# Kernel optimization log

Measured on AMD Instinct MI355X. Metric: run time of the kernel, lower is better.

The kernel has to match this reference:

```python
import jax, jax.numpy as jnp
import numpy as np

N = 4096        # batch size (rows)
K = 4           # instances per class -> num_instances in the torch code
D = 256         # embedding dim
MARGIN = 0.5
SAMPLE_KEY = jax.random.key(42)  # fixed key: deterministic stand-in for torch.multinomial


def setup_inputs() -> dict:
    key = jax.random.key(0)
    x = jax.random.normal(key, (N, D), dtype=jnp.float32)
    # L2-normalize like typical metric-learning embeddings so sims are in [-1, 1]
    inputs = x / jnp.linalg.norm(x, axis=1, keepdims=True)
    targets = (jnp.arange(N) // K).astype(jnp.int32)  # P*K batch: equal-size classes
    return {"inputs": inputs, "targets": targets}


def reference(inputs, targets):
    n = inputs.shape[0]
    km1 = K - 1                 # positives per row
    n_neg = n - K               # negatives per row

    sim = inputs @ inputs.T                                   # [n, n]
    same = targets[:, None] == targets[None, :]
    eye = jnp.eye(n, dtype=bool)
    pos_mask = same & ~eye
    neg_mask = ~same

    # masked_select + per-row sort: masked entries -> +inf, ascending sort,
    # keep first count entries (counts are uniform across rows)
    pos_sorted = jnp.sort(jnp.where(pos_mask, sim, jnp.inf), axis=1)[:, :km1]   # [n, K-1]
    neg_sorted = jnp.sort(jnp.where(neg_mask, sim, jnp.inf), axis=1)[:, :n_neg] # [n, n-K]

    pos_d = jnp.mean(pos_sorted)
    neg_d = jnp.mean(neg_sorted)

    # GaussDistribution per row over negatives
    neg_mean = jnp.mean(neg_sorted, axis=1, keepdims=True)
    neg_std = jnp.sqrt(jnp.mean((neg_sorted - neg_mean) ** 2, axis=1, keepdims=True))
    # NOTE: the original uses exp(+(x-mu)^2 / (2 sigma^2)) (no minus sign) -- faithful
    logprob = (neg_sorted - neg_mean) ** 2 / (2.0 * neg_std ** 2)               # [n, n-K]

    # multinomial without replacement ~ Gumbel top-k on log-weights
    gumbel = -jnp.log(-jnp.log(
        jax.random.uniform(SAMPLE_KEY, logprob.shape, minval=1e-20, maxval=1.0)))
    _, neg_idx = jax.lax.top_k(logprob + gumbel, km1)                            # [n, K-1]
    neg_pair = jnp.take_along_axis(neg_sorted, neg_idx, axis=1)                  # [n, K-1]

    pos_loss = jnp.mean(jnp.log1p(jnp.exp(-2.0 * (pos_sorted - MARGIN))), axis=1)
    neg_loss = 0.04 * jnp.mean(jnp.log1p(jnp.exp(50.0 * (neg_pair - MARGIN))), axis=1)
    loss = jnp.sum(pos_loss + neg_loss) / n

    # prec: fraction of rows where hardest positive > hardest sampled negative + 0.05
    c = jnp.sum(pos_sorted[:, -1] > jnp.max(neg_pair, axis=1) + 0.05)
    prec = c.astype(jnp.float32) / n

    return loss, prec, pos_d, neg_d
```

## Files before the change

kernel.cpp:

```cpp
#include <hip/hip_runtime.h>
#include <hip/hip_bf16.h>
#include <cstdint>
#include <cfloat>
#include <math.h>

#define NN 4096
#define DD 256
#define NNEG 4092
#define MARGIN 0.5f
#define NB 3584
#define NW (NB / 2)

__device__ __forceinline__ uint32_t rotl32(uint32_t x, int r) {
  return (x << r) | (x >> (32 - r));
}

__device__ __forceinline__ void threefry2x32_42(uint32_t x0, uint32_t x1,
                                                uint32_t& o0, uint32_t& o1) {
  const uint32_t k0 = 0u, k1 = 42u;
  const uint32_t k2 = k0 ^ k1 ^ 0x1BD11BDAu;
  x0 += k0; x1 += k1;
#define TF_R(r) { x0 += x1; x1 = rotl32(x1, r); x1 ^= x0; }
  TF_R(13) TF_R(15) TF_R(26) TF_R(6)
  x0 += k1; x1 += k2 + 1u;
  TF_R(17) TF_R(29) TF_R(16) TF_R(24)
  x0 += k2; x1 += k0 + 2u;
  TF_R(13) TF_R(15) TF_R(26) TF_R(6)
  x0 += k0; x1 += k1 + 3u;
  TF_R(17) TF_R(29) TF_R(16) TF_R(24)
  x0 += k1; x1 += k2 + 4u;
  TF_R(13) TF_R(15) TF_R(26) TF_R(6)
  x0 += k2; x1 += k0 + 5u;
#undef TF_R
  o0 = x0; o1 = x1;
}

__device__ __forceinline__ float gumbel_at(uint32_t f) {
  uint32_t o0, o1;
  threefry2x32_42(0u, f, o0, o1);
  uint32_t bits = o0 ^ o1;
  uint32_t fb = (bits >> 9) | 0x3F800000u;
  float fl = __uint_as_float(fb) - 1.0f;
  float u = fmaxf(1e-20f, fl + 1e-20f);
  return -__logf(-__logf(u));
}

__device__ __forceinline__ int bucket_of(float v) {
  return (int)fminf(fmaxf((v + 0.5f) * (float)NB, 0.0f), (float)(NB - 1));
}

#define BT 64
#define NT (NN / BT)
#define BK 32
#define LDSS 36

__global__ __launch_bounds__(256) void gemm_sim(const float* __restrict__ X,
                                                float* __restrict__ S) {
  __shared__ float As[BT * LDSS];
  __shared__ float Bs[BT * LDSS];
  const int tid = threadIdx.x;
  const int tx = tid & 15, ty = tid >> 4;

  int b = blockIdx.x, bi = 0;
  while (b >= NT - bi) { b -= NT - bi; bi++; }
  const int bj = bi + b;
  const int rowBase = bi * BT, colBase = bj * BT;

  float acc[4][4] = {};
  for (int kb = 0; kb < DD; kb += BK) {
#pragma unroll
    for (int it = 0; it < 2; ++it) {
      int idx = tid + 256 * it;
      int r = idx >> 3, c4 = idx & 7;
      float4 av = *(const float4*)(X + (size_t)(rowBase + r) * DD + kb + c4 * 4);
      float4 bv = *(const float4*)(X + (size_t)(colBase + r) * DD + kb + c4 * 4);
      *(float4*)(As + r * LDSS + c4 * 4) = av;
      *(float4*)(Bs + r * LDSS + c4 * 4) = bv;
    }
    __syncthreads();
    for (int k = 0; k < BK; k += 4) {
      float4 a[4], bfr[4];
#pragma unroll
      for (int i = 0; i < 4; ++i) a[i] = *(const float4*)(As + (ty + 16 * i) * LDSS + k);
#pragma unroll
      for (int j = 0; j < 4; ++j) bfr[j] = *(const float4*)(Bs + (tx + 16 * j) * LDSS + k);
#pragma unroll
      for (int i = 0; i < 4; ++i)
#pragma unroll
        for (int j = 0; j < 4; ++j) {
          acc[i][j] += a[i].x * bfr[j].x;
          acc[i][j] += a[i].y * bfr[j].y;
          acc[i][j] += a[i].z * bfr[j].z;
          acc[i][j] += a[i].w * bfr[j].w;
        }
    }
    __syncthreads();
  }
#pragma unroll
  for (int i = 0; i < 4; ++i)
#pragma unroll
    for (int j = 0; j < 4; ++j)
      S[(size_t)(rowBase + ty + 16 * i) * NN + colBase + tx + 16 * j] = acc[i][j];
  if (bi != bj) {
#pragma unroll
    for (int i = 0; i < 4; ++i)
#pragma unroll
      for (int j = 0; j < 4; ++j)
        S[(size_t)(colBase + tx + 16 * j) * NN + rowBase + ty + 16 * i] = acc[i][j];
  }
}

#define INSERT3(sc, v)                                              \
  if ((sc) > s2) {                                                  \
    if ((sc) > s1) {                                                \
      s2 = s1; v2 = v1;                                             \
      if ((sc) > s0) { s1 = s0; v1 = v0; s0 = (sc); v0 = (v); }     \
      else           { s1 = (sc); v1 = (v); }                       \
    } else { s2 = (sc); v2 = (v); }                                 \
  }

__global__ __launch_bounds__(256) void row_kernel(const float* __restrict__ S,
                                                  float* __restrict__ acc) {
  __shared__ uint32_t histw[NW];
  __shared__ float sval[NN];
  __shared__ float sh[48];
  __shared__ uint32_t wtot[4];

  const int row = blockIdx.x;
  const int tid = threadIdx.x;
  const int lane = tid & 63, wid = tid >> 6;

#pragma unroll
  for (int i = 0; i < 7; ++i) histw[tid + 256 * i] = 0u;

  const float4* src = (const float4*)(S + (size_t)row * NN);
  const int pslot = row >> 2;
  float vv[16];
#pragma unroll
  for (int it = 0; it < 4; ++it) {
    int slot = tid + 256 * it;
    float4 t4 = src[slot];
    if (slot == pslot) {
      sh[16] = t4.x; sh[17] = t4.y; sh[18] = t4.z; sh[19] = t4.w;
      t4.x = INFINITY; t4.y = INFINITY; t4.z = INFINITY; t4.w = INFINITY;
    }
    vv[4 * it + 0] = t4.x; vv[4 * it + 1] = t4.y;
    vv[4 * it + 2] = t4.z; vv[4 * it + 3] = t4.w;
  }

  float s = 0.0f;
#pragma unroll
  for (int e = 0; e < 16; ++e) if (vv[e] < 1e30f) s += vv[e];
#pragma unroll
  for (int off = 32; off > 0; off >>= 1) s += __shfl_down(s, off, 64);
  if (lane == 0) sh[5 + wid] = s;
  __syncthreads();

#pragma unroll
  for (int e = 0; e < 16; ++e) {
    int b = bucket_of(vv[e]);
    atomicAdd(&histw[b >> 1], 1u << ((b & 1) << 4));
  }
  if (tid == 0) {
    int self = row & 3;
    float p[3]; int m = 0;
#pragma unroll
    for (int c = 0; c < 4; ++c)
      if (c != self) p[m++] = sh[16 + c];
    float t;
    if (p[0] > p[1]) { t = p[0]; p[0] = p[1]; p[1] = t; }
    if (p[1] > p[2]) { t = p[1]; p[1] = p[2]; p[2] = t; }
    if (p[0] > p[1]) { t = p[0]; p[0] = p[1]; p[1] = t; }
    sh[0] = p[0]; sh[1] = p[1]; sh[2] = p[2];
    float tot = sh[5] + sh[6] + sh[7] + sh[8];
    sh[9] = tot;
    sh[3] = tot / (float)NNEG;
  }
  __syncthreads();

  uint32_t hw[7];
  uint32_t s14 = 0;
#pragma unroll
  for (int j = 0; j < 7; ++j) {
    hw[j] = histw[7 * tid + j];
    s14 += (hw[j] & 0xFFFFu) + (hw[j] >> 16);
  }
  uint32_t inc = s14;
#pragma unroll
  for (int off = 1; off < 64; off <<= 1) {
    uint32_t n = __shfl_up(inc, (unsigned)off, 64);
    if (lane >= off) inc += n;
  }
  if (lane == 63) wtot[wid] = inc;

  const float mu = sh[3];
  float q = 0.0f;
#pragma unroll
  for (int e = 0; e < 16; ++e)
    if (vv[e] < 1e30f) { float d = vv[e] - mu; q += d * d; }
#pragma unroll
  for (int off = 32; off > 0; off >>= 1) q += __shfl_down(q, off, 64);
  if (lane == 0) sh[10 + wid] = q;
  __syncthreads();

  uint32_t wbase = 0;
  for (int w = 0; w < wid; ++w) wbase += wtot[w];
  uint32_t run = wbase + inc - s14;
#pragma unroll
  for (int j = 0; j < 7; ++j) {
    uint32_t lo = run; run += hw[j] & 0xFFFFu;
    uint32_t hi = run; run += hw[j] >> 16;
    histw[7 * tid + j] = lo | (hi << 16);
  }
  if (tid == 0) {
    float var = (sh[10] + sh[11] + sh[12] + sh[13]) / (float)NNEG;
    float sd = sqrtf(var);
    sh[4] = 1.0f / (2.0f * sd * sd);
  }
  __syncthreads();

#pragma unroll
  for (int e = 0; e < 16; ++e) {
    int b = bucket_of(vv[e]);
    uint32_t old = atomicAdd(&histw[b >> 1], 1u << ((b & 1) << 4));
    uint32_t sl = (old >> ((b & 1) << 4)) & 0xFFFFu;
    sval[sl] = vv[e];
  }
  __syncthreads();

  const float inv2s2 = sh[4];
  const uint32_t fbase = (uint32_t)row * (uint32_t)NNEG;
  float s0 = -FLT_MAX, s1 = -FLT_MAX, s2 = -FLT_MAX;
  float v0 = 0.0f, v1 = 0.0f, v2 = 0.0f;
#pragma unroll 1
  for (int it = 0; it < 16; ++it) {
    int sl = tid + 256 * it;
    float v = sval[sl];
    if (v < 1e30f) {
      int b = bucket_of(v);
      uint32_t w = histw[b >> 1];
      uint32_t end, st;
      if (b & 1) { end = w >> 16; st = w & 0xFFFFu; }
      else {
        end = w & 0xFFFFu;
        st = (b == 0) ? 0u : (histw[(b >> 1) - 1] >> 16);
      }
      int cnt = (int)st;
      for (uint32_t u = st; u < end; ++u) {
        float wv = sval[u];
        cnt += (wv < v || (wv == v && (int)u < sl)) ? 1 : 0;
      }
      float d = v - mu;
      float sc = d * d * inv2s2 + gumbel_at(fbase + (uint32_t)cnt);
      INSERT3(sc, v)
    }
  }

#pragma unroll
  for (int dlt = 1; dlt < 64; dlt <<= 1) {
    float t0 = __shfl_xor(s0, dlt, 64), u0 = __shfl_xor(v0, dlt, 64);
    float t1 = __shfl_xor(s1, dlt, 64), u1 = __shfl_xor(v1, dlt, 64);
    float t2 = __shfl_xor(s2, dlt, 64), u2 = __shfl_xor(v2, dlt, 64);
    INSERT3(t0, u0)
    INSERT3(t1, u1)
    INSERT3(t2, u2)
  }
  if (lane == 0) {
    int b0 = 24 + wid * 6;
    sh[b0 + 0] = s0; sh[b0 + 1] = v0;
    sh[b0 + 2] = s1; sh[b0 + 3] = v1;
    sh[b0 + 4] = s2; sh[b0 + 5] = v2;
  }
  __syncthreads();

  if (tid == 0) {
    float g0 = -FLT_MAX, g1 = -FLT_MAX, g2 = -FLT_MAX;
    float w0 = 0.0f, w1 = 0.0f, w2 = 0.0f;
    {
      float s0 = g0, s1 = g1, s2 = g2, v0 = w0, v1 = w1, v2 = w2;
#pragma unroll
      for (int i = 0; i < 12; ++i) {
        float sc = sh[24 + 2 * i], v = sh[24 + 2 * i + 1];
        INSERT3(sc, v)
      }
      g0 = s0; g1 = s1; g2 = s2; w0 = v0; w1 = v1; w2 = v2;
    }
    float negmax = fmaxf(w0, fmaxf(w1, w2));
    float neg_loss = 0.04f * (log1pf(expf(50.0f * (w0 - MARGIN))) +
                              log1pf(expf(50.0f * (w1 - MARGIN))) +
                              log1pf(expf(50.0f * (w2 - MARGIN)))) / 3.0f;
    float p0 = sh[0], p1 = sh[1], p2 = sh[2];
    float pos_loss = (log1pf(expf(-2.0f * (p0 - MARGIN))) +
                      log1pf(expf(-2.0f * (p1 - MARGIN))) +
                      log1pf(expf(-2.0f * (p2 - MARGIN)))) / 3.0f;
    atomicAdd(&acc[0], pos_loss + neg_loss);
    if (p2 > negmax + 0.05f) atomicAdd(&acc[1], 1.0f);
    atomicAdd(&acc[2], p0 + p1 + p2);
    atomicAdd(&acc[3], sh[9]);
  }
}

__global__ void finalize(const float* __restrict__ acc, float* out) {
  if (threadIdx.x == 0 && blockIdx.x == 0) {
    out[0] = acc[0] / 4096.0f;
    out[1] = acc[1] / 4096.0f;
    out[2] = acc[2] / (4096.0f * 3.0f);
    out[3] = acc[3] / (4096.0f * 4092.0f);
  }
}

extern "C" void kernel_launch(void* const* d_in, const int* in_sizes, int n_in,
                              void* d_out, int out_size, void* d_ws, size_t ws_size,
                              hipStream_t stream) {
  (void)in_sizes; (void)n_in; (void)out_size; (void)ws_size;
  const float* X = (const float*)d_in[0];
  float* S = (float*)d_ws;
  float* acc = (float*)((char*)d_ws + (size_t)NN * NN * 4);
  hipMemsetAsync(acc, 0, 4 * sizeof(float), stream);
  gemm_sim<<<NT * (NT + 1) / 2, 256, 0, stream>>>(X, S);
  row_kernel<<<NN, 256, 0, stream>>>(S, acc);
  finalize<<<1, 64, 0, stream>>>(acc, (float*)d_out);
}
```

Measured before the change: 375.3 us.

## Enlarge GEMM per-thread tile to 8x8 and batch rank-counting loads in row kernel

The similarity GEMM now uses 64-thread blocks, with each thread computing an 8x8 output micro-tile instead of 4x4. This raises register-level reuse of the LDS fragments but cuts threads per block and raises register pressure. The row kernel's rank/score loop is split into three phases: load values, compute bucket ranges, then count ranks with 8-wide batched LDS reads, followed by the Gumbel scoring. This exposes more memory-level parallelism at the cost of extra registers.

```diff
diff --git a/kernel.cpp b/kernel.cpp
--- a/kernel.cpp
+++ b/kernel.cpp
@@ -54,23 +54,23 @@
 #define BK 32
 #define LDSS 36
 
-__global__ __launch_bounds__(256) void gemm_sim(const float* __restrict__ X,
-                                                float* __restrict__ S) {
+__global__ __launch_bounds__(64) void gemm_sim(const float* __restrict__ X,
+                                               float* __restrict__ S) {
   __shared__ float As[BT * LDSS];
   __shared__ float Bs[BT * LDSS];
-  const int tid = threadIdx.x;
-  const int tx = tid & 15, ty = tid >> 4;
+  const int lane = threadIdx.x;
+  const int tx = lane & 7, ty = lane >> 3;
 
   int b = blockIdx.x, bi = 0;
   while (b >= NT - bi) { b -= NT - bi; bi++; }
   const int bj = bi + b;
   const int rowBase = bi * BT, colBase = bj * BT;
 
-  float acc[4][4] = {};
+  float acc[8][8] = {};
   for (int kb = 0; kb < DD; kb += BK) {
 #pragma unroll
-    for (int it = 0; it < 2; ++it) {
-      int idx = tid + 256 * it;
+    for (int it = 0; it < 8; ++it) {
+      int idx = lane + 64 * it;
       int r = idx >> 3, c4 = idx & 7;
       float4 av = *(const float4*)(X + (size_t)(rowBase + r) * DD + kb + c4 * 4);
       float4 bv = *(const float4*)(X + (size_t)(colBase + r) * DD + kb + c4 * 4);
@@ -78,16 +78,17 @@
       *(float4*)(Bs + r * LDSS + c4 * 4) = bv;
     }
     __syncthreads();
+#pragma unroll
     for (int k = 0; k < BK; k += 4) {
-      float4 a[4], bfr[4];
-#pragma unroll
-      for (int i = 0; i < 4; ++i) a[i] = *(const float4*)(As + (ty + 16 * i) * LDSS + k);
-#pragma unroll
-      for (int j = 0; j < 4; ++j) bfr[j] = *(const float4*)(Bs + (tx + 16 * j) * LDSS + k);
-#pragma unroll
-      for (int i = 0; i < 4; ++i)
-#pragma unroll
-        for (int j = 0; j < 4; ++j) {
+      float4 a[8], bfr[8];
+#pragma unroll
+      for (int i = 0; i < 8; ++i) a[i] = *(const float4*)(As + (ty + 8 * i) * LDSS + k);
+#pragma unroll
+      for (int j = 0; j < 8; ++j) bfr[j] = *(const float4*)(Bs + (tx + 8 * j) * LDSS + k);
+#pragma unroll
+      for (int i = 0; i < 8; ++i)
+#pragma unroll
+        for (int j = 0; j < 8; ++j) {
           acc[i][j] += a[i].x * bfr[j].x;
           acc[i][j] += a[i].y * bfr[j].y;
           acc[i][j] += a[i].z * bfr[j].z;
@@ -97,16 +98,16 @@
     __syncthreads();
   }
 #pragma unroll
-  for (int i = 0; i < 4; ++i)
-#pragma unroll
-    for (int j = 0; j < 4; ++j)
-      S[(size_t)(rowBase + ty + 16 * i) * NN + colBase + tx + 16 * j] = acc[i][j];
+  for (int i = 0; i < 8; ++i)
+#pragma unroll
+    for (int j = 0; j < 8; ++j)
+      S[(size_t)(rowBase + ty + 8 * i) * NN + colBase + tx + 8 * j] = acc[i][j];
   if (bi != bj) {
 #pragma unroll
-    for (int i = 0; i < 4; ++i)
-#pragma unroll
-      for (int j = 0; j < 4; ++j)
-        S[(size_t)(colBase + tx + 16 * j) * NN + rowBase + ty + 16 * i] = acc[i][j];
+    for (int i = 0; i < 8; ++i)
+#pragma unroll
+      for (int j = 0; j < 8; ++j)
+        S[(size_t)(colBase + tx + 8 * j) * NN + rowBase + ty + 8 * i] = acc[i][j];
   }
 }
 
@@ -228,14 +229,15 @@
   }
   __syncthreads();
 
-  const float inv2s2 = sh[4];
-  const uint32_t fbase = (uint32_t)row * (uint32_t)NNEG;
-  float s0 = -FLT_MAX, s1 = -FLT_MAX, s2 = -FLT_MAX;
-  float v0 = 0.0f, v1 = 0.0f, v2 = 0.0f;
-#pragma unroll 1
+  float v16[16];
+#pragma unroll
+  for (int it = 0; it < 16; ++it) v16[it] = sval[tid + 256 * it];
+
+  uint32_t stend[16];
+#pragma unroll
   for (int it = 0; it < 16; ++it) {
-    int sl = tid + 256 * it;
-    float v = sval[sl];
+    float v = v16[it];
+    uint32_t se = 0;
     if (v < 1e30f) {
       int b = bucket_of(v);
       uint32_t w = histw[b >> 1];
@@ -245,13 +247,48 @@
         end = w & 0xFFFFu;
         st = (b == 0) ? 0u : (histw[(b >> 1) - 1] >> 16);
       }
-      int cnt = (int)st;
-      for (uint32_t u = st; u < end; ++u) {
-        float wv = sval[u];
-        cnt += (wv < v || (wv == v && (int)u < sl)) ? 1 : 0;
+      se = st | (end << 16);
+    }
+    stend[it] = se;
+  }
+
+  int rk[16];
+#pragma unroll 2
+  for (int it = 0; it < 16; ++it) {
+    uint32_t st = stend[it] & 0xFFFFu, end = stend[it] >> 16;
+    float v = v16[it];
+    int sl = tid + 256 * it;
+    int cnt = (int)st;
+    uint32_t u = st;
+    while (u < end) {
+      float w8[8]; uint32_t i8[8];
+#pragma unroll
+      for (int t = 0; t < 8; ++t) {
+        uint32_t uu = u + t;
+        uint32_t x = (uu < end) ? uu : (uint32_t)sl;
+        i8[t] = x;
+        w8[t] = sval[x];
       }
+#pragma unroll
+      for (int t = 0; t < 8; ++t) {
+        float wv = w8[t];
+        cnt += (wv < v || (wv == v && (int)i8[t] < sl)) ? 1 : 0;
+      }
+      u += 8;
+    }
+    rk[it] = cnt;
+  }
+
+  const float inv2s2 = sh[4];
+  const uint32_t fbase = (uint32_t)row * (uint32_t)NNEG;
+  float s0 = -FLT_MAX, s1 = -FLT_MAX, s2 = -FLT_MAX;
+  float v0 = 0.0f, v1 = 0.0f, v2 = 0.0f;
+#pragma unroll 4
+  for (int it = 0; it < 16; ++it) {
+    float v = v16[it];
+    if (v < 1e30f) {
       float d = v - mu;
-      float sc = d * d * inv2s2 + gumbel_at(fbase + (uint32_t)cnt);
+      float sc = d * d * inv2s2 + gumbel_at(fbase + (uint32_t)rk[it]);
       INSERT3(sc, v)
     }
   }
@@ -317,7 +354,7 @@
   float* S = (float*)d_ws;
   float* acc = (float*)((char*)d_ws + (size_t)NN * NN * 4);
   hipMemsetAsync(acc, 0, 4 * sizeof(float), stream);
-  gemm_sim<<<NT * (NT + 1) / 2, 256, 0, stream>>>(X, S);
+  gemm_sim<<<NT * (NT + 1) / 2, 64, 0, stream>>>(X, S);
   row_kernel<<<NN, 256, 0, stream>>>(S, acc);
   finalize<<<1, 64, 0, stream>>>(acc, (float*)d_out);
 }
```

Result: slower. 391.0 us (+4.2%).
